# Performance work log

Measured on AMD Instinct MI355X. Metric: run time of the kernel, lower is better.

## Reference

```python
import jax, jax.numpy as jnp
import numpy as np

NUM_ANCHORS = 3
NUM_CLASSES = 80
STRIDES = (16.0, 32.0)
ANCHORS = (
    jnp.array([[12.64, 19.39], [37.88, 51.48], [55.71, 138.31]], dtype=jnp.float32),
    jnp.array([[126.91, 78.23], [131.57, 214.55], [279.92, 258.87]], dtype=jnp.float32),
)


def conv1x1(x, w, b):
    # x: [B,C,H,W], w: [O,C], b: [O] -> [B,O,H,W]
    return jnp.einsum('bchw,oc->bohw', x, w) + b[None, :, None, None]


def decode_level(reg, obj, cls, stride, anchors):
    # reg: [B,12,H,W], obj: [B,3,H,W], cls: [B,80,H,W]
    B, _, H, W = reg.shape
    r = reg.transpose(0, 2, 3, 1).reshape(B, H, W, NUM_ANCHORS, 4)
    o = obj.transpose(0, 2, 3, 1).reshape(B, H, W, NUM_ANCHORS, 1)
    c = cls.transpose(0, 2, 3, 1)[:, :, :, None, :]  # [B,H,W,1,80], shared across anchors
    gy, gx = jnp.meshgrid(jnp.arange(H, dtype=reg.dtype), jnp.arange(W, dtype=reg.dtype), indexing='ij')
    grid = jnp.stack([gx, gy], axis=-1)[None, :, :, None, :]  # [1,H,W,1,2] = (x, y)
    xy = (jax.nn.sigmoid(r[..., :2]) * 2.0 - 0.5 + grid) * stride
    wh = (jax.nn.sigmoid(r[..., 2:4]) * 2.0) ** 2 * anchors  # anchors [3,2] broadcast
    ob = jax.nn.sigmoid(o)
    cp = jnp.broadcast_to(jax.nn.softmax(c, axis=-1), (B, H, W, NUM_ANCHORS, NUM_CLASSES))
    boxes = jnp.concatenate([xy, wh, ob, cp], axis=-1)  # [B,H,W,3,85]
    return boxes.reshape(B, H * W * NUM_ANCHORS, 5 + NUM_CLASSES)


def setup_inputs() -> dict:
    key = jax.random.key(0)
    ks = jax.random.split(key, 12)
    B, C = 64, 72
    inp = {
        'feat_reg0': jax.random.normal(ks[0], (B, C, 40, 40), jnp.float32),
        'feat_obj0': jax.random.normal(ks[1], (B, C, 40, 40), jnp.float32),
        'feat_cls0': jax.random.normal(ks[2], (B, C, 40, 40), jnp.float32),
        'feat_reg1': jax.random.normal(ks[3], (B, C, 20, 20), jnp.float32),
        'feat_obj1': jax.random.normal(ks[4], (B, C, 20, 20), jnp.float32),
        'feat_cls1': jax.random.normal(ks[5], (B, C, 20, 20), jnp.float32),
        'w_reg': jax.random.normal(ks[6], (4 * NUM_ANCHORS, C), jnp.float32) * 0.05,
        'b_reg': jax.random.normal(ks[7], (4 * NUM_ANCHORS,), jnp.float32) * 0.05,
        'w_obj': jax.random.normal(ks[8], (NUM_ANCHORS, C), jnp.float32) * 0.05,
        'b_obj': jax.random.normal(ks[9], (NUM_ANCHORS,), jnp.float32) * 0.05,
        'w_cls': jax.random.normal(ks[10], (NUM_CLASSES, C), jnp.float32) * 0.05,
        'b_cls': jax.random.normal(ks[11], (NUM_CLASSES,), jnp.float32) * 0.05,
    }
    return inp


def reference(feat_reg0, feat_obj0, feat_cls0, feat_reg1, feat_obj1, feat_cls1,
              w_reg, b_reg, w_obj, b_obj, w_cls, b_cls):
    feats = ((feat_reg0, feat_obj0, feat_cls0), (feat_reg1, feat_obj1, feat_cls1))
    outs = []
    for i, (fr, fo, fc) in enumerate(feats):
        reg = conv1x1(fr, w_reg, b_reg)
        obj = conv1x1(fo, w_obj, b_obj)
        cls = conv1x1(fc, w_cls, b_cls)
        outs.append(decode_level(reg, obj, cls, STRIDES[i], ANCHORS[i]))
    return jnp.concatenate(outs, axis=1)  # [B, 6000, 85]
```

## Files before the change

### kernel.cpp

```cpp
#include <hip/hip_runtime.h>
#include <math.h>

#define BLOCK 256
#define NPOS 64
#define C_IN 72
#define AST 102
#define ASTI 51
#define TSZ (NPOS * AST)
#define RST 100
#define NFRAG 21

typedef short short8  __attribute__((ext_vector_type(8)));
typedef float floatx4 __attribute__((ext_vector_type(4)));

__device__ __forceinline__ unsigned short f2bf(float f) {
    unsigned u = __float_as_uint(f);
    u += 0x7FFFu + ((u >> 16) & 1u);
    return (unsigned short)(u >> 16);
}
__device__ __forceinline__ float sigf(float x) {
    return __builtin_amdgcn_rcpf(1.0f + __expf(-x));
}

__global__ void __launch_bounds__(BLOCK)
build_bfrags_kernel(const float* __restrict__ w_reg,
                    const float* __restrict__ w_obj,
                    const float* __restrict__ w_cls,
                    short8* __restrict__ frags)
{
    int idx = blockIdx.x * BLOCK + threadIdx.x;
    if (idx >= NFRAG * 64) return;
    int lane = idx & 63;
    int fi   = idx >> 6;
    int tile = fi / 3, kc = fi - tile * 3;
    int m = lane & 15, quad = lane >> 4;
    const float* wrow;
    bool valid = true;
    if (tile == 0)      { wrow = w_reg + m * C_IN; valid = (m < 12); }
    else if (tile == 1) { wrow = w_obj + m * C_IN; valid = (m < 3); }
    else                { wrow = w_cls + ((tile - 2) * 16 + m) * C_IN; }
    short8 r = {0, 0, 0, 0, 0, 0, 0, 0};
    if (valid && !(kc == 2 && quad != 0)) {
        const float* p = wrow + kc * 32 + quad * 8;
#pragma unroll
        for (int j = 0; j < 8; ++j) r[j] = (short)f2bf(p[j]);
    }
    frags[fi * 64 + lane] = r;
}

__global__ void __launch_bounds__(BLOCK, 3)
yolo_head_kernel(const float* __restrict__ fr0, const float* __restrict__ fo0, const float* __restrict__ fc0,
                 const float* __restrict__ fr1, const float* __restrict__ fo1, const float* __restrict__ fc1,
                 const float* __restrict__ b_reg, const float* __restrict__ b_obj,
                 const float* __restrict__ b_cls,
                 const short8* __restrict__ wfrag,
                 float* __restrict__ out)
{
    __shared__ __align__(16) short sA[3 * TSZ];
    float* row = (float*)sA;

    const int bid  = blockIdx.x;
    const int tid  = threadIdx.x;
    const int lane = tid & 63;
    const int wv   = tid >> 6;
    const int m    = lane & 15;
    const int quad = lane >> 4;

    int lvl, b, pos0, HW, W, LO;
    const float *fr, *fo, *fc;
    if (bid < 1600) {
        lvl = 0; b = bid / 25; pos0 = (bid % 25) * NPOS;
        HW = 1600; W = 40; LO = 0; fr = fr0; fo = fo0; fc = fc0;
    } else {
        int t = bid - 1600;
        lvl = 1; b = t / 7; pos0 = (t % 7) * NPOS;
        HW = 400; W = 20; LO = 4800; fr = fr1; fo = fo1; fc = fc1;
    }
    const float STRIDE = lvl ? 32.0f : 16.0f;
    const int active = (HW - pos0 < NPOS) ? (HW - pos0) : NPOS;
    const int pos    = pos0 + lane;
    const int posc   = (pos < HW) ? pos : (HW - 1);

    short8 bf[NFRAG];
#pragma unroll
    for (int i = 0; i < NFRAG; ++i) bf[i] = wfrag[i * 64 + lane];

    {
        int* sAi = (int*)sA;
        const float* srcs[3] = {fr, fo, fc};
#pragma unroll
        for (int t = 0; t < 3; ++t) {
            const float* sp = srcs[t] + b * C_IN * HW + posc;
            int* dp = sAi + t * (TSZ / 2) + lane * ASTI;
            float lf[18];
#pragma unroll
            for (int i = 0; i < 9; ++i) {
                int c0 = wv * 2 + i * 8;
                lf[2 * i]     = sp[c0 * HW];
                lf[2 * i + 1] = sp[(c0 + 1) * HW];
            }
#pragma unroll
            for (int i = 0; i < 18; ++i)
                asm volatile("" : "+v"(lf[i]));
#pragma unroll
            for (int i = 0; i < 9; ++i) {
                int c0 = wv * 2 + i * 8;
                dp[c0 >> 1] = (int)f2bf(lf[2 * i]) | ((int)f2bf(lf[2 * i + 1]) << 16);
            }
        }
#pragma unroll
        for (int i = 0; i < NFRAG; ++i)
            asm volatile("" : "+v"(*(floatx4*)&bf[i]));
        for (int i = tid; i < 3 * NPOS * 15; i += BLOCK) {
            int t = i / (NPOS * 15), r = i - t * (NPOS * 15);
            int p = r / 15, s = r - p * 15;
            sAi[t * (TSZ / 2) + p * ASTI + 36 + s] = 0;
        }
    }
    __syncthreads();

    const int mt = wv;
    auto afrag = [&](int t, int kc) -> short8 {
        return *reinterpret_cast<const short8*>(
            sA + t * TSZ + (mt * 16 + m) * AST + kc * 32 + quad * 8);
    };

    floatx4 accR = {0, 0, 0, 0}, accO = {0, 0, 0, 0}, accC[5];
#pragma unroll
    for (int kc = 0; kc < 3; ++kc)
        accR = __builtin_amdgcn_mfma_f32_16x16x32_bf16(afrag(0, kc), bf[0 * 3 + kc], accR, 0, 0, 0);
#pragma unroll
    for (int kc = 0; kc < 3; ++kc)
        accO = __builtin_amdgcn_mfma_f32_16x16x32_bf16(afrag(1, kc), bf[1 * 3 + kc], accO, 0, 0, 0);
#pragma unroll
    for (int nt = 0; nt < 5; ++nt) {
        floatx4 a4 = {0, 0, 0, 0};
#pragma unroll
        for (int kc = 0; kc < 3; ++kc)
            a4 = __builtin_amdgcn_mfma_f32_16x16x32_bf16(afrag(2, kc), bf[(nt + 2) * 3 + kc], a4, 0, 0, 0);
        accC[nt] = a4;
    }

    __syncthreads();

#pragma unroll
    for (int i = 0; i < 4; ++i) {
        int pl = mt * 16 + quad * 4 + i;
        if (m < 12) row[pl * RST + m]      = accR[i] + b_reg[m];
        if (m < 3)  row[pl * RST + 12 + m] = accO[i] + b_obj[m];
    }
#pragma unroll
    for (int nt = 0; nt < 5; ++nt) {
        float bc = b_cls[nt * 16 + m];
#pragma unroll
        for (int i = 0; i < 4; ++i) {
            int pl = mt * 16 + quad * 4 + i;
            row[pl * RST + 15 + nt * 16 + m] = __expf(accC[nt][i] + bc);
        }
    }
    __syncthreads();

    if (tid < NPOS) {
        float* rr = row + tid * RST;
        float s = rr[15] + rr[92] + rr[93] + rr[94];
#pragma unroll
        for (int i2 = 4; i2 < 23; ++i2) {
            floatx4 e4 = *reinterpret_cast<const floatx4*>(rr + i2 * 4);
            s += (e4[0] + e4[1]) + (e4[2] + e4[3]);
        }
        rr[95] = __builtin_amdgcn_rcpf(s);

        float r12[12], ob3[3];
#pragma unroll
        for (int j = 0; j < 12; ++j) r12[j] = rr[j];
#pragma unroll
        for (int a = 0; a < 3; ++a) ob3[a] = rr[12 + a];

        int pg = pos0 + tid; if (pg >= HW) pg = HW - 1;
        const int gyi = lvl ? (pg / 20) : (pg / 40);
        const float gx = (float)(pg - gyi * W);
        const float gy = (float)gyi;
        float A[6];
        if (lvl == 0) { A[0]=12.64f;  A[1]=19.39f;  A[2]=37.88f;  A[3]=51.48f;  A[4]=55.71f;  A[5]=138.31f; }
        else          { A[0]=126.91f; A[1]=78.23f;  A[2]=131.57f; A[3]=214.55f; A[4]=279.92f; A[5]=258.87f; }
#pragma unroll
        for (int a = 0; a < 3; ++a) {
            float x  = (sigf(r12[4*a + 0]) * 2.0f - 0.5f + gx) * STRIDE;
            float y  = (sigf(r12[4*a + 1]) * 2.0f - 0.5f + gy) * STRIDE;
            float tw = sigf(r12[4*a + 2]) * 2.0f;
            float th = sigf(r12[4*a + 3]) * 2.0f;
            rr[a*5 + 0] = x;
            rr[a*5 + 1] = y;
            rr[a*5 + 2] = tw * tw * A[2*a + 0];
            rr[a*5 + 3] = th * th * A[2*a + 1];
            rr[a*5 + 4] = sigf(ob3[a]);
        }
    }
    __syncthreads();

    int wi[4], wflag[4];
#pragma unroll
    for (int j = 0; j < 4; ++j) {
        int f = lane + 64 * j;
        int k = (f > 254) ? 0 : f;
        int a  = (k >= 85) + (k >= 170);
        int kk = k - a * 85;
        wi[j]    = (kk < 5) ? (a * 5 + kk) : (15 + (kk - 5));
        wflag[j] = (kk >= 5);
    }
    float* outp = out + (b * 510000 + LO * 85 + pos0 * 255);

    for (int p = wv; p < active; p += 4) {
        const float* rr = row + p * RST;
        float inv = rr[95];
        float* po = outp + p * 255 + lane;
#pragma unroll
        for (int j = 0; j < 4; ++j) {
            if (!(lane == 63 && j == 3)) {
                float v = rr[wi[j]];
                if (wflag[j]) v *= inv;
                po[64 * j] = v;
            }
        }
    }
}

extern "C" void kernel_launch(void* const* d_in, const int* in_sizes, int n_in,
                              void* d_out, int out_size, void* d_ws, size_t ws_size,
                              hipStream_t stream) {
    (void)in_sizes; (void)n_in; (void)ws_size; (void)out_size;
    const float* fr0  = (const float*)d_in[0];
    const float* fo0  = (const float*)d_in[1];
    const float* fc0  = (const float*)d_in[2];
    const float* fr1  = (const float*)d_in[3];
    const float* fo1  = (const float*)d_in[4];
    const float* fc1  = (const float*)d_in[5];
    const float* wreg = (const float*)d_in[6];
    const float* breg = (const float*)d_in[7];
    const float* wobj = (const float*)d_in[8];
    const float* bobj = (const float*)d_in[9];
    const float* wcls = (const float*)d_in[10];
    const float* bcls = (const float*)d_in[11];
    float* out = (float*)d_out;
    short8* frags = (short8*)d_ws;

    build_bfrags_kernel<<<6, BLOCK, 0, stream>>>(wreg, wobj, wcls, frags);

    yolo_head_kernel<<<2048, BLOCK, 0, stream>>>(
        fr0, fo0, fc0, fr1, fo1, fc1,
        breg, bobj, bcls, frags, out);
}
```

Measured before the change: 248.9 us.

## Use single-wave blocks of 16 positions with register A-fragments and shuffle softmax

Restructures the head kernel so each 64-thread block handles 16 positions. A-fragments are loaded from global memory directly into MFMA registers instead of being staged through LDS. The decode and softmax now run in the MFMA accumulator layout, with the softmax sum reduced via 16-lane shuffles, which removes several block barriers and the serial per-position pass. The cost is a 4x larger grid, more weight-fragment reloads per block, and narrower coalesced input loads of 16 floats per channel row.

```diff
diff --git a/kernel.cpp b/kernel.cpp
--- a/kernel.cpp
+++ b/kernel.cpp
@@ -1,13 +1,8 @@
 #include <hip/hip_runtime.h>
 #include <math.h>
 
-#define BLOCK 256
-#define NPOS 64
 #define C_IN 72
-#define AST 102
-#define ASTI 51
-#define TSZ (NPOS * AST)
-#define RST 100
+#define RST 97
 #define NFRAG 21
 
 typedef short short8  __attribute__((ext_vector_type(8)));
@@ -22,13 +17,13 @@
     return __builtin_amdgcn_rcpf(1.0f + __expf(-x));
 }
 
-__global__ void __launch_bounds__(BLOCK)
+__global__ void __launch_bounds__(256)
 build_bfrags_kernel(const float* __restrict__ w_reg,
                     const float* __restrict__ w_obj,
                     const float* __restrict__ w_cls,
                     short8* __restrict__ frags)
 {
-    int idx = blockIdx.x * BLOCK + threadIdx.x;
+    int idx = blockIdx.x * 256 + threadIdx.x;
     if (idx >= NFRAG * 64) return;
     int lane = idx & 63;
     int fi   = idx >> 6;
@@ -48,7 +43,7 @@
     frags[fi * 64 + lane] = r;
 }
 
-__global__ void __launch_bounds__(BLOCK, 3)
+__global__ void __launch_bounds__(64, 4)
 yolo_head_kernel(const float* __restrict__ fr0, const float* __restrict__ fo0, const float* __restrict__ fc0,
                  const float* __restrict__ fr1, const float* __restrict__ fo1, const float* __restrict__ fc1,
                  const float* __restrict__ b_reg, const float* __restrict__ b_obj,
@@ -56,171 +51,142 @@
                  const short8* __restrict__ wfrag,
                  float* __restrict__ out)
 {
-    __shared__ __align__(16) short sA[3 * TSZ];
-    float* row = (float*)sA;
-
+    __shared__ __align__(16) float row[16 * RST];
     const int bid  = blockIdx.x;
-    const int tid  = threadIdx.x;
-    const int lane = tid & 63;
-    const int wv   = tid >> 6;
+    const int lane = threadIdx.x;
     const int m    = lane & 15;
     const int quad = lane >> 4;
 
     int lvl, b, pos0, HW, W, LO;
     const float *fr, *fo, *fc;
-    if (bid < 1600) {
-        lvl = 0; b = bid / 25; pos0 = (bid % 25) * NPOS;
+    if (bid < 6400) {
+        lvl = 0; b = bid / 100; pos0 = (bid - b * 100) * 16;
         HW = 1600; W = 40; LO = 0; fr = fr0; fo = fo0; fc = fc0;
     } else {
-        int t = bid - 1600;
-        lvl = 1; b = t / 7; pos0 = (t % 7) * NPOS;
+        int t = bid - 6400;
+        lvl = 1; b = t / 25; pos0 = (t - b * 25) * 16;
         HW = 400; W = 20; LO = 4800; fr = fr1; fo = fo1; fc = fc1;
     }
     const float STRIDE = lvl ? 32.0f : 16.0f;
-    const int active = (HW - pos0 < NPOS) ? (HW - pos0) : NPOS;
-    const int pos    = pos0 + lane;
-    const int posc   = (pos < HW) ? pos : (HW - 1);
-
-    short8 bf[NFRAG];
-#pragma unroll
-    for (int i = 0; i < NFRAG; ++i) bf[i] = wfrag[i * 64 + lane];
-
-    {
-        int* sAi = (int*)sA;
-        const float* srcs[3] = {fr, fo, fc};
-#pragma unroll
-        for (int t = 0; t < 3; ++t) {
-            const float* sp = srcs[t] + b * C_IN * HW + posc;
-            int* dp = sAi + t * (TSZ / 2) + lane * ASTI;
-            float lf[18];
-#pragma unroll
-            for (int i = 0; i < 9; ++i) {
-                int c0 = wv * 2 + i * 8;
-                lf[2 * i]     = sp[c0 * HW];
-                lf[2 * i + 1] = sp[(c0 + 1) * HW];
-            }
-#pragma unroll
-            for (int i = 0; i < 18; ++i)
-                asm volatile("" : "+v"(lf[i]));
-#pragma unroll
-            for (int i = 0; i < 9; ++i) {
-                int c0 = wv * 2 + i * 8;
-                dp[c0 >> 1] = (int)f2bf(lf[2 * i]) | ((int)f2bf(lf[2 * i + 1]) << 16);
-            }
-        }
-#pragma unroll
-        for (int i = 0; i < NFRAG; ++i)
-            asm volatile("" : "+v"(*(floatx4*)&bf[i]));
-        for (int i = tid; i < 3 * NPOS * 15; i += BLOCK) {
-            int t = i / (NPOS * 15), r = i - t * (NPOS * 15);
-            int p = r / 15, s = r - p * 15;
-            sAi[t * (TSZ / 2) + p * ASTI + 36 + s] = 0;
-        }
-    }
-    __syncthreads();
-
-    const int mt = wv;
-    auto afrag = [&](int t, int kc) -> short8 {
-        return *reinterpret_cast<const short8*>(
-            sA + t * TSZ + (mt * 16 + m) * AST + kc * 32 + quad * 8);
-    };
+
+    const int fbase = b * C_IN * HW + pos0 + m;
+    short8 af[3][3];
+    const float* srcs[3] = {fr, fo, fc};
+#pragma unroll
+    for (int t = 0; t < 3; ++t) {
+        const float* sp = srcs[t] + fbase;
+        float lf[16];
+#pragma unroll
+        for (int kc = 0; kc < 2; ++kc)
+#pragma unroll
+            for (int j = 0; j < 8; ++j)
+                lf[kc * 8 + j] = sp[(kc * 32 + quad * 8 + j) * HW];
+        float l2[8] = {0, 0, 0, 0, 0, 0, 0, 0};
+        if (quad == 0) {
+#pragma unroll
+            for (int j = 0; j < 8; ++j) l2[j] = sp[(64 + j) * HW];
+        }
+#pragma unroll
+        for (int kc = 0; kc < 2; ++kc) {
+            short8 r;
+#pragma unroll
+            for (int j = 0; j < 8; ++j) r[j] = (short)f2bf(lf[kc * 8 + j]);
+            af[t][kc] = r;
+        }
+        short8 r2 = {0, 0, 0, 0, 0, 0, 0, 0};
+        if (quad == 0) {
+#pragma unroll
+            for (int j = 0; j < 8; ++j) r2[j] = (short)f2bf(l2[j]);
+        }
+        af[t][2] = r2;
+    }
 
     floatx4 accR = {0, 0, 0, 0}, accO = {0, 0, 0, 0}, accC[5];
 #pragma unroll
     for (int kc = 0; kc < 3; ++kc)
-        accR = __builtin_amdgcn_mfma_f32_16x16x32_bf16(afrag(0, kc), bf[0 * 3 + kc], accR, 0, 0, 0);
+        accR = __builtin_amdgcn_mfma_f32_16x16x32_bf16(af[0][kc], wfrag[(0 * 3 + kc) * 64 + lane], accR, 0, 0, 0);
 #pragma unroll
     for (int kc = 0; kc < 3; ++kc)
-        accO = __builtin_amdgcn_mfma_f32_16x16x32_bf16(afrag(1, kc), bf[1 * 3 + kc], accO, 0, 0, 0);
+        accO = __builtin_amdgcn_mfma_f32_16x16x32_bf16(af[1][kc], wfrag[(1 * 3 + kc) * 64 + lane], accO, 0, 0, 0);
 #pragma unroll
     for (int nt = 0; nt < 5; ++nt) {
         floatx4 a4 = {0, 0, 0, 0};
 #pragma unroll
         for (int kc = 0; kc < 3; ++kc)
-            a4 = __builtin_amdgcn_mfma_f32_16x16x32_bf16(afrag(2, kc), bf[(nt + 2) * 3 + kc], a4, 0, 0, 0);
+            a4 = __builtin_amdgcn_mfma_f32_16x16x32_bf16(af[2][kc], wfrag[((nt + 2) * 3 + kc) * 64 + lane], a4, 0, 0, 0);
         accC[nt] = a4;
     }
 
-    __syncthreads();
+    const int a_ = m >> 2, k_ = m & 3;
+    float anch;
+    {
+        float e0, e1;
+        if (lvl == 0) { e0 = a_ == 0 ? 12.64f  : a_ == 1 ? 37.88f  : 55.71f;
+                        e1 = a_ == 0 ? 19.39f  : a_ == 1 ? 51.48f  : 138.31f; }
+        else          { e0 = a_ == 0 ? 126.91f : a_ == 1 ? 131.57f : 279.92f;
+                        e1 = a_ == 0 ? 78.23f  : a_ == 1 ? 214.55f : 258.87f; }
+        anch = (k_ == 3) ? e1 : e0;
+    }
+    const float brg = b_reg[m < 12 ? m : 0];
+    const float bob = b_obj[m < 3 ? m : 0];
+    float bcl[5];
+#pragma unroll
+    for (int nt = 0; nt < 5; ++nt) bcl[nt] = b_cls[nt * 16 + m];
 
 #pragma unroll
     for (int i = 0; i < 4; ++i) {
-        int pl = mt * 16 + quad * 4 + i;
-        if (m < 12) row[pl * RST + m]      = accR[i] + b_reg[m];
-        if (m < 3)  row[pl * RST + 12 + m] = accO[i] + b_obj[m];
-    }
-#pragma unroll
-    for (int nt = 0; nt < 5; ++nt) {
-        float bc = b_cls[nt * 16 + m];
-#pragma unroll
-        for (int i = 0; i < 4; ++i) {
-            int pl = mt * 16 + quad * 4 + i;
-            row[pl * RST + 15 + nt * 16 + m] = __expf(accC[nt][i] + bc);
-        }
-    }
-    __syncthreads();
-
-    if (tid < NPOS) {
-        float* rr = row + tid * RST;
-        float s = rr[15] + rr[92] + rr[93] + rr[94];
-#pragma unroll
-        for (int i2 = 4; i2 < 23; ++i2) {
-            floatx4 e4 = *reinterpret_cast<const floatx4*>(rr + i2 * 4);
-            s += (e4[0] + e4[1]) + (e4[2] + e4[3]);
-        }
-        rr[95] = __builtin_amdgcn_rcpf(s);
-
-        float r12[12], ob3[3];
-#pragma unroll
-        for (int j = 0; j < 12; ++j) r12[j] = rr[j];
-#pragma unroll
-        for (int a = 0; a < 3; ++a) ob3[a] = rr[12 + a];
-
-        int pg = pos0 + tid; if (pg >= HW) pg = HW - 1;
-        const int gyi = lvl ? (pg / 20) : (pg / 40);
+        const int prel = quad * 4 + i;
+        const int pg   = pos0 + prel;
+        const int gyi  = lvl ? (pg / 20) : (pg / 40);
         const float gx = (float)(pg - gyi * W);
         const float gy = (float)gyi;
-        float A[6];
-        if (lvl == 0) { A[0]=12.64f;  A[1]=19.39f;  A[2]=37.88f;  A[3]=51.48f;  A[4]=55.71f;  A[5]=138.31f; }
-        else          { A[0]=126.91f; A[1]=78.23f;  A[2]=131.57f; A[3]=214.55f; A[4]=279.92f; A[5]=258.87f; }
-#pragma unroll
-        for (int a = 0; a < 3; ++a) {
-            float x  = (sigf(r12[4*a + 0]) * 2.0f - 0.5f + gx) * STRIDE;
-            float y  = (sigf(r12[4*a + 1]) * 2.0f - 0.5f + gy) * STRIDE;
-            float tw = sigf(r12[4*a + 2]) * 2.0f;
-            float th = sigf(r12[4*a + 3]) * 2.0f;
-            rr[a*5 + 0] = x;
-            rr[a*5 + 1] = y;
-            rr[a*5 + 2] = tw * tw * A[2*a + 0];
-            rr[a*5 + 3] = th * th * A[2*a + 1];
-            rr[a*5 + 4] = sigf(ob3[a]);
-        }
+
+        if (m < 12) {
+            float sg = sigf(accR[i] + brg);
+            float v;
+            if (k_ == 0)      v = (sg * 2.0f - 0.5f + gx) * STRIDE;
+            else if (k_ == 1) v = (sg * 2.0f - 0.5f + gy) * STRIDE;
+            else { float t2 = sg * 2.0f; v = t2 * t2 * anch; }
+            row[prel * RST + a_ * 5 + k_] = v;
+        }
+        if (m < 3)
+            row[prel * RST + m * 5 + 4] = sigf(accO[i] + bob);
+
+        float e[5];
+        float s = 0.f;
+#pragma unroll
+        for (int nt = 0; nt < 5; ++nt) {
+            e[nt] = __expf(accC[nt][i] + bcl[nt]);
+            s += e[nt];
+        }
+        s += __shfl_xor(s, 1, 16);
+        s += __shfl_xor(s, 2, 16);
+        s += __shfl_xor(s, 4, 16);
+        s += __shfl_xor(s, 8, 16);
+        const float inv = __builtin_amdgcn_rcpf(s);
+#pragma unroll
+        for (int nt = 0; nt < 5; ++nt)
+            row[prel * RST + 15 + nt * 16 + m] = e[nt] * inv;
     }
     __syncthreads();
 
-    int wi[4], wflag[4];
+    int wi0[4];
 #pragma unroll
     for (int j = 0; j < 4; ++j) {
         int f = lane + 64 * j;
         int k = (f > 254) ? 0 : f;
         int a  = (k >= 85) + (k >= 170);
         int kk = k - a * 85;
-        wi[j]    = (kk < 5) ? (a * 5 + kk) : (15 + (kk - 5));
-        wflag[j] = (kk >= 5);
-    }
-    float* outp = out + (b * 510000 + LO * 85 + pos0 * 255);
-
-    for (int p = wv; p < active; p += 4) {
+        wi0[j] = (kk < 5) ? (a * 5 + kk) : (15 + (kk - 5));
+    }
+    float* outp = out + ((size_t)b * 510000 + LO * 85 + pos0 * 255);
+    for (int p = 0; p < 16; ++p) {
         const float* rr = row + p * RST;
-        float inv = rr[95];
         float* po = outp + p * 255 + lane;
 #pragma unroll
         for (int j = 0; j < 4; ++j) {
-            if (!(lane == 63 && j == 3)) {
-                float v = rr[wi[j]];
-                if (wflag[j]) v *= inv;
-                po[64 * j] = v;
-            }
+            if (!(lane == 63 && j == 3))
+                po[64 * j] = rr[wi0[j]];
         }
     }
 }
@@ -244,9 +210,9 @@
     float* out = (float*)d_out;
     short8* frags = (short8*)d_ws;
 
-    build_bfrags_kernel<<<6, BLOCK, 0, stream>>>(wreg, wobj, wcls, frags);
-
-    yolo_head_kernel<<<2048, BLOCK, 0, stream>>>(
+    build_bfrags_kernel<<<6, 256, 0, stream>>>(wreg, wobj, wcls, frags);
+
+    yolo_head_kernel<<<8000, 64, 0, stream>>>(
         fr0, fo0, fc0, fr1, fo1, fc1,
         breg, bobj, bcls, frags, out);
 }
```

Result: no change. 247.0 us (-0.7%).
